# Optimization experiments

Hardware: AMD Instinct MI355X
Metric: run time of the kernel (lower is better)

The kernel has to match this reference:

```python
import jax, jax.numpy as jnp
import numpy as np

HEADS = 16

def setup_inputs() -> dict:
    key = jax.random.key(0)
    ks = jax.random.split(key, 5)
    B, N, D = 2, 2048, 1024
    q = jax.random.normal(ks[0], (B, N, D), dtype=jnp.float32)
    kv = jax.random.normal(ks[1], (B, N, D), dtype=jnp.float32)
    # nn.Linear default init scale ~ 1/sqrt(fan_in); use scaled normals
    s = 1.0 / np.sqrt(D)
    Wq = jax.random.normal(ks[2], (D, D), dtype=jnp.float32) * s
    Wkv = jax.random.normal(ks[3], (D, 2 * D), dtype=jnp.float32) * s
    Wout = jax.random.normal(ks[4], (D, D), dtype=jnp.float32) * s
    return {"q": q, "kv": kv, "Wq": Wq, "Wkv": Wkv, "Wout": Wout}

def reference(q, kv, Wq, Wkv, Wout):
    B, N, D = q.shape
    H = HEADS
    Dh = D // H
    scale = Dh ** -0.5
    # projections (Linear, no bias); weights stored [in, out]
    qp = q @ Wq                      # [B,N,D]
    kvp = kv @ Wkv                   # [B,N,2D]
    kp, vp = kvp[..., :D], kvp[..., D:]
    def split_heads(t):
        return t.reshape(B, N, H, Dh).transpose(0, 2, 1, 3)  # [B,H,N,Dh]
    qh, kh, vh = split_heads(qp), split_heads(kp), split_heads(vp)
    dots = jnp.einsum('bhid,bhjd->bhij', qh, kh) * scale
    # attn_fn = softmax computed in float32, cast back to input dtype
    attn = jax.nn.softmax(dots.astype(jnp.float32), axis=-1).astype(dots.dtype)
    out = jnp.einsum('bhij,bhjd->bhid', attn, vh)
    out = out.transpose(0, 2, 1, 3).reshape(B, N, D)
    return out @ Wout
```

## Files before the change

kernel.cpp:

```cpp
#include <hip/hip_runtime.h>
#include <hip/hip_fp16.h>
#include <stdint.h>

using u16 = unsigned short;
using f16   = _Float16;
using fp16v2 = __attribute__((ext_vector_type(2))) __fp16;
using f16x4 = __attribute__((ext_vector_type(4))) _Float16;
using f16x8 = __attribute__((ext_vector_type(8))) _Float16;
using f32x4 = __attribute__((ext_vector_type(4))) float;

__device__ __forceinline__ u16 f2h(float f) {
  union { f16 h; u16 u; } v;
  v.h = (f16)f;
  return v.u;
}

#define GLOBAL_LOAD_LDS16(gp, lp) \
  __builtin_amdgcn_global_load_lds((const __attribute__((address_space(1))) unsigned int*)(gp), \
                                   (__attribute__((address_space(3))) unsigned int*)(lp), 16, 0, 0)

#define MFMA32(a, b, c) __builtin_amdgcn_mfma_f32_16x16x32_f16(a, b, c, 0, 0, 0)
#define MFMA16(a, b, c) __builtin_amdgcn_mfma_f32_16x16x16f16(a, b, c, 0, 0, 0)

__global__ __launch_bounds__(256) void cast2_f16_k(const float4* __restrict__ a,
                                                   const float4* __restrict__ b,
                                                   u16* __restrict__ outa,
                                                   u16* __restrict__ outb, int n4each) {
  int i = blockIdx.x * 256 + threadIdx.x;
  const float4* src; u16* dst; int j;
  if (i < n4each) { src = a; dst = outa; j = i; }
  else            { src = b; dst = outb; j = i - n4each; }
  float4 f = src[j];
  ushort4 o;
  o.x = f2h(f.x); o.y = f2h(f.y); o.z = f2h(f.z); o.w = f2h(f.w);
  *(ushort4*)(dst + (size_t)j * 4) = o;
}

__global__ __launch_bounds__(256) void transpose3_k(const float* __restrict__ Wq,
                                                    const float* __restrict__ Wkv,
                                                    const float* __restrict__ Wout,
                                                    u16* __restrict__ WqT,
                                                    u16* __restrict__ WkvT,
                                                    u16* __restrict__ WoutT,
                                                    float qscale) {
  int blk = blockIdx.x;
  const float* in; u16* out; int t; float scale; int N;
  if (blk < 1024)      { in = Wq;   out = WqT;   t = blk;        scale = qscale; N = 1024; }
  else if (blk < 3072) { in = Wkv;  out = WkvT;  t = blk - 1024; scale = 1.0f;   N = 2048; }
  else                 { in = Wout; out = WoutT; t = blk - 3072; scale = 1.0f;   N = 1024; }
  const int K = 1024;
  __shared__ float tile[32][33];
  int bk = (t & 31) * 32, bn = (t >> 5) * 32;
  int tx = threadIdx.x & 31, ty = threadIdx.x >> 5;
#pragma unroll
  for (int i = 0; i < 4; i++) {
    int r = ty * 4 + i;
    tile[r][tx] = in[(size_t)(bk + r) * N + bn + tx];
  }
  __syncthreads();
#pragma unroll
  for (int i = 0; i < 4; i++) {
    int r = ty * 4 + i;
    out[(size_t)(bn + r) * K + bk + tx] = f2h(tile[tx][r] * scale);
  }
}

template <int BM, bool OUT_F32>
__device__ __forceinline__ void gemm_body(u16* lA, u16* lB,
                                          const u16* __restrict__ A, const u16* __restrict__ BT,
                                          void* __restrict__ Cv, int N, int K, int bm, int bn) {
  const int tid = threadIdx.x;
  const int lane = tid & 63, wave = tid >> 6;
  const int l15 = lane & 15, quad = lane >> 4;
  constexpr int MI = BM / 32;
  const int wm = (wave >> 1) * (BM / 2), wn = (wave & 1) * 64;

  f32x4 acc[MI][4] = {};

  const u16* Abase = A + (size_t)bm * BM * K;
  const u16* Bbase = BT + (size_t)bn * 128 * K;
  const int r0 = tid >> 2, c8 = (tid & 3) * 8;

  u16* lAw = lA + wave * 512;
  u16* lBw = lB + wave * 512;

  for (int k0 = 0; k0 < K; k0 += 32) {
    const u16* Ag = Abase + k0 + (size_t)r0 * K + c8;
    const u16* Bg = Bbase + k0 + (size_t)r0 * K + c8;
#pragma unroll
    for (int t = 0; t < BM / 64; t++)
      GLOBAL_LOAD_LDS16(Ag + (size_t)(t * 64) * K, lAw + t * 2048);
#pragma unroll
    for (int t = 0; t < 2; t++)
      GLOBAL_LOAD_LDS16(Bg + (size_t)(t * 64) * K, lBw + t * 2048);
    __syncthreads();

    f16x8 aF[MI], bF[4];
#pragma unroll
    for (int mi = 0; mi < MI; mi++)
      aF[mi] = *(const f16x8*)&lA[(wm + mi * 16 + l15) * 32 + quad * 8];
#pragma unroll
    for (int ni = 0; ni < 4; ni++)
      bF[ni] = *(const f16x8*)&lB[(wn + ni * 16 + l15) * 32 + quad * 8];
    __builtin_amdgcn_s_setprio(1);
#pragma unroll
    for (int mi = 0; mi < MI; mi++)
#pragma unroll
      for (int ni = 0; ni < 4; ni++)
        acc[mi][ni] = MFMA32(aF[mi], bF[ni], acc[mi][ni]);
    __builtin_amdgcn_s_setprio(0);
    __syncthreads();
  }

  const int col0 = bn * 128 + wn + l15;
  const int rowb = bm * BM + wm + quad * 4;
#pragma unroll
  for (int mi = 0; mi < MI; mi++) {
#pragma unroll
    for (int ni = 0; ni < 4; ni++) {
#pragma unroll
      for (int r = 0; r < 4; r++) {
        int row = rowb + mi * 16 + r;
        int col = col0 + ni * 16;
        float v = acc[mi][ni][r];
        if (OUT_F32) ((float*)Cv)[(size_t)row * N + col] = v;
        else         ((u16*)Cv)[(size_t)row * N + col] = f2h(v);
      }
    }
  }
}

__global__ __launch_bounds__(256) void proj_k(const u16* __restrict__ q16, const u16* __restrict__ WqT,
                                              u16* __restrict__ qp,
                                              const u16* __restrict__ kv16, const u16* __restrict__ WkvT,
                                              u16* __restrict__ kvp) {
  __shared__ u16 lA[128 * 32];
  __shared__ u16 lB[128 * 32];
  int blk = blockIdx.x;
  if (blk < 256) gemm_body<128, false>(lA, lB, q16, WqT, qp, 1024, 1024, blk >> 3, blk & 7);
  else { int b2 = blk - 256; gemm_body<128, false>(lA, lB, kv16, WkvT, kvp, 2048, 1024, b2 >> 4, b2 & 15); }
}

__global__ __launch_bounds__(256) void gemm_out_k(const u16* __restrict__ A, const u16* __restrict__ BT,
                                                  float* __restrict__ C) {
  __shared__ u16 lA[64 * 32];
  __shared__ u16 lB[128 * 32];
  int blk = blockIdx.x;
  gemm_body<64, true>(lA, lB, A, BT, C, 1024, 1024, blk >> 3, blk & 7);
}

__global__ __launch_bounds__(256) void vt_k(const u16* __restrict__ kvp,
                                            u16* __restrict__ VT) {
  __shared__ u16 lT[64 * 64];
  const int jt = blockIdx.x & 31;
  const int bh = blockIdx.x >> 5;
  const int b = bh >> 4, h = bh & 15;
  const int j0 = jt * 64;
  const int u = threadIdx.x;
  const int su = u >> 3;
  const int sc = (u & 7) * 8;

#pragma unroll
  for (int t = 0; t < 2; t++) {
    int j = su + t * 32;
    int s = (j ^ (j >> 3)) & 7;
    uint4 vv = *(const uint4*)(kvp + (size_t)(b * 2048 + j0 + j) * 2048 + 1024 + h * 64 + sc);
    *(uint4*)&lT[j * 64 + (sc ^ (s << 3))] = vv;
  }
  __syncthreads();

  const int jg = u & 7;
#pragma unroll
  for (int t = 0; t < 2; t++) {
    int d = su + t * 32;
    u16 tmp[8];
#pragma unroll
    for (int i = 0; i < 8; i++) {
      int j = jg * 8 + i;
      int s = (j ^ (j >> 3)) & 7;
      tmp[i] = lT[j * 64 + (d ^ (s << 3))];
    }
    *(uint4*)(VT + ((size_t)bh * 64 + d) * 2048 + j0 + jg * 8) = *(const uint4*)tmp;
  }
}

__global__ __launch_bounds__(256) void flash_attn_k(const u16* __restrict__ qp,
                                                    const u16* __restrict__ kvp,
                                                    const u16* __restrict__ VT,
                                                    u16* __restrict__ attn_out) {
  const int NSEQ = 2048, D = 1024, LDKV = 2048;
  const int mtile = blockIdx.x & 15;
  const int bh = blockIdx.x >> 4;
  const int b = bh >> 4, h = bh & 15;
  const int tid = threadIdx.x;
  const int lane = tid & 63, wave = tid >> 6;
  const int quad = lane >> 4, l15 = lane & 15;

  __shared__ u16 lK[2][128 * 64];
  __shared__ u16 lV[2][64 * 128];

  const u16* Qb  = qp + (size_t)(b * NSEQ + mtile * 128) * D + h * 64;
  const u16* Kb  = kvp + (size_t)(b * NSEQ) * LDKV + h * 64;
  const u16* VTb = VT + (size_t)bh * 64 * 2048;

  f16x8 qa[2][2];
#pragma unroll
  for (int qt = 0; qt < 2; qt++)
#pragma unroll
    for (int ks = 0; ks < 2; ks++)
      qa[qt][ks] = *(const f16x8*)(Qb + (size_t)(wave * 32 + qt * 16 + l15) * D + ks * 32 + quad * 8);

  f32x4 oacc[2][4] = {};
  float rs0 = 0.f, rs1 = 0.f;

#define STAGEB(LKB, LVB, J0)                                                        \
  {                                                                                 \
    u16* lKw_ = (LKB) + wave * 512;                                                 \
    u16* lVw_ = (LVB) + wave * 512;                                                 \
    _Pragma("unroll")                                                               \
    for (int t = 0; t < 4; t++) {                                                   \
      int g = t * 256 + tid;                                                        \
      int jr = g >> 3;                                                              \
      int c = (g & 7) ^ (jr & 7);                                                   \
      GLOBAL_LOAD_LDS16(Kb + (size_t)((J0) + jr) * LDKV + c * 8, lKw_ + t * 2048);  \
    }                                                                               \
    _Pragma("unroll")                                                               \
    for (int t = 0; t < 4; t++) {                                                   \
      int g = t * 256 + tid;                                                        \
      int d = g >> 4;                                                               \
      int c = (g & 15) ^ (d & 7);                                                   \
      GLOBAL_LOAD_LDS16(VTb + (size_t)d * 2048 + (J0) + c * 8, lVw_ + t * 2048);    \
    }                                                                               \
  }

  STAGEB(lK[0], lV[0], 0);

  for (int it = 0; it < 16; it++) {
    const int cur = it & 1;
    __syncthreads();
    if (it < 15) STAGEB(lK[cur ^ 1], lV[cur ^ 1], (it + 1) * 128);

    const u16* lKc = lK[cur];
    const u16* lVc = lV[cur];

#pragma unroll
    for (int ni = 0; ni < 8; ni++) {
      f32x4 s0 = f32x4{-4.f, -4.f, -4.f, -4.f};
      f32x4 s1 = s0;
      __builtin_amdgcn_s_setprio(1);
#pragma unroll
      for (int ks = 0; ks < 2; ks++) {
        int p = ((ks * 4 + quad) ^ (l15 & 7)) * 8;
        f16x8 kb = *(const f16x8*)&lKc[(ni * 16 + l15) * 64 + p];
        s0 = MFMA32(kb, qa[0][ks], s0);
        s1 = MFMA32(kb, qa[1][ks], s1);
      }
      __builtin_amdgcn_s_setprio(0);

      union { fp16v2 h2[2]; f16x4 v; } pa0, pa1;
      {
        float p0 = __builtin_amdgcn_exp2f(s0[0]);
        float p1 = __builtin_amdgcn_exp2f(s0[1]);
        float p2 = __builtin_amdgcn_exp2f(s0[2]);
        float p3 = __builtin_amdgcn_exp2f(s0[3]);
        rs0 += (p0 + p1) + (p2 + p3);
        pa0.h2[0] = __builtin_amdgcn_cvt_pkrtz(p0, p1);
        pa0.h2[1] = __builtin_amdgcn_cvt_pkrtz(p2, p3);
      }
      {
        float p0 = __builtin_amdgcn_exp2f(s1[0]);
        float p1 = __builtin_amdgcn_exp2f(s1[1]);
        float p2 = __builtin_amdgcn_exp2f(s1[2]);
        float p3 = __builtin_amdgcn_exp2f(s1[3]);
        rs1 += (p0 + p1) + (p2 + p3);
        pa1.h2[0] = __builtin_amdgcn_cvt_pkrtz(p0, p1);
        pa1.h2[1] = __builtin_amdgcn_cvt_pkrtz(p2, p3);
      }

      __builtin_amdgcn_s_setprio(1);
#pragma unroll
      for (int di = 0; di < 4; di++) {
        int p = (((2 * ni + (quad >> 1)) ^ (l15 & 7)) * 8) + (quad & 1) * 4;
        f16x4 vb = *(const f16x4*)&lVc[(di * 16 + l15) * 128 + p];
        oacc[0][di] = MFMA16(pa0.v, vb, oacc[0][di]);
        oacc[1][di] = MFMA16(pa1.v, vb, oacc[1][di]);
      }
      __builtin_amdgcn_s_setprio(0);
    }
  }

  rs0 += __shfl_xor(rs0, 16, 64);
  rs0 += __shfl_xor(rs0, 32, 64);
  rs1 += __shfl_xor(rs1, 16, 64);
  rs1 += __shfl_xor(rs1, 32, 64);
  float inv0 = 1.0f / rs0;
  float inv1 = 1.0f / rs1;
  float invq0[4], invq1[4];
#pragma unroll
  for (int r = 0; r < 4; r++) {
    int src = (lane & 48) + ((lane >> 4) << 2) + r;
    invq0[r] = __shfl(inv0, src, 64);
    invq1[r] = __shfl(inv1, src, 64);
  }

  u16* Ob = attn_out + (size_t)(b * NSEQ + mtile * 128) * D + h * 64;
#pragma unroll
  for (int di = 0; di < 4; di++)
#pragma unroll
    for (int r = 0; r < 4; r++) {
      float v0 = oacc[0][di][r] * invq0[r];
      float v1 = oacc[1][di][r] * invq1[r];
      Ob[(size_t)(wave * 32 + quad * 4 + r) * D + di * 16 + l15] = f2h(v0);
      Ob[(size_t)(wave * 32 + 16 + quad * 4 + r) * D + di * 16 + l15] = f2h(v1);
    }
}

extern "C" void kernel_launch(void* const* d_in, const int* in_sizes, int n_in,
                              void* d_out, int out_size, void* d_ws, size_t ws_size,
                              hipStream_t stream) {
  const float* q    = (const float*)d_in[0];
  const float* kv   = (const float*)d_in[1];
  const float* Wq   = (const float*)d_in[2];
  const float* Wkv  = (const float*)d_in[3];
  const float* Wout = (const float*)d_in[4];
  float* out = (float*)d_out;

  char* ws = (char*)d_ws;
  const size_t MB = 1024 * 1024;
  u16* q16   = (u16*)(ws + 0);
  u16* kv16  = (u16*)(ws + 8 * MB);
  u16* WqT   = (u16*)(ws + 16 * MB);
  u16* WkvT  = (u16*)(ws + 18 * MB);
  u16* WoutT = (u16*)(ws + 22 * MB);
  u16* qp    = (u16*)(ws + 24 * MB);
  u16* kvp   = (u16*)(ws + 32 * MB);
  u16* attn  = q16;
  u16* VT    = kv16;

  const float qscale = 0.125f * 1.44269504f;

  cast2_f16_k<<<8192, 256, 0, stream>>>((const float4*)q, (const float4*)kv,
                                        q16, kv16, 1048576);
  transpose3_k<<<4096, 256, 0, stream>>>(Wq, Wkv, Wout, WqT, WkvT, WoutT, qscale);

  proj_k<<<768, 256, 0, stream>>>(q16, WqT, qp, kv16, WkvT, kvp);
  vt_k<<<1024, 256, 0, stream>>>(kvp, VT);
  flash_attn_k<<<512, 256, 0, stream>>>(qp, kvp, VT, attn);
  gemm_out_k<<<512, 256, 0, stream>>>(attn, WoutT, out);
}
```

Measured before the change: 213.6 us.

## Fuse V transpose into KV projection epilogue and merge prep kernels

The KV projection GEMM now writes the V half directly in transposed per-head layout, which removes the separate vt_k kernel and its read and write of V. K is stored compactly with stride 1024. The cast and weight-transpose kernels are merged into a single launch, which removes one kernel launch. The s_setprio hints around the MFMA loop are dropped. The transposed V stores are 8-byte writes strided across rows, so they may coalesce poorly.

```diff
diff --git a/kernel.cpp b/kernel.cpp
--- a/kernel.cpp
+++ b/kernel.cpp
@@ -22,34 +22,34 @@
 #define MFMA32(a, b, c) __builtin_amdgcn_mfma_f32_16x16x32_f16(a, b, c, 0, 0, 0)
 #define MFMA16(a, b, c) __builtin_amdgcn_mfma_f32_16x16x16f16(a, b, c, 0, 0, 0)
 
-__global__ __launch_bounds__(256) void cast2_f16_k(const float4* __restrict__ a,
-                                                   const float4* __restrict__ b,
-                                                   u16* __restrict__ outa,
-                                                   u16* __restrict__ outb, int n4each) {
-  int i = blockIdx.x * 256 + threadIdx.x;
-  const float4* src; u16* dst; int j;
-  if (i < n4each) { src = a; dst = outa; j = i; }
-  else            { src = b; dst = outb; j = i - n4each; }
-  float4 f = src[j];
-  ushort4 o;
-  o.x = f2h(f.x); o.y = f2h(f.y); o.z = f2h(f.z); o.w = f2h(f.w);
-  *(ushort4*)(dst + (size_t)j * 4) = o;
-}
-
-__global__ __launch_bounds__(256) void transpose3_k(const float* __restrict__ Wq,
-                                                    const float* __restrict__ Wkv,
-                                                    const float* __restrict__ Wout,
-                                                    u16* __restrict__ WqT,
-                                                    u16* __restrict__ WkvT,
-                                                    u16* __restrict__ WoutT,
-                                                    float qscale) {
+__global__ __launch_bounds__(256) void prep_k(const float4* __restrict__ q,
+                                              const float4* __restrict__ kv,
+                                              u16* __restrict__ q16, u16* __restrict__ kv16,
+                                              const float* __restrict__ Wq,
+                                              const float* __restrict__ Wkv,
+                                              const float* __restrict__ Wout,
+                                              u16* __restrict__ WqT, u16* __restrict__ WkvT,
+                                              u16* __restrict__ WoutT, float qscale) {
+  __shared__ float tile[32][33];
   int blk = blockIdx.x;
+  if (blk < 8192) {
+    int i = blk * 256 + threadIdx.x;
+    const int n4each = 1048576;
+    const float4* src; u16* dst; int j;
+    if (i < n4each) { src = q;  dst = q16;  j = i; }
+    else            { src = kv; dst = kv16; j = i - n4each; }
+    float4 f = src[j];
+    ushort4 o;
+    o.x = f2h(f.x); o.y = f2h(f.y); o.z = f2h(f.z); o.w = f2h(f.w);
+    *(ushort4*)(dst + (size_t)j * 4) = o;
+    return;
+  }
+  int t2 = blk - 8192;
   const float* in; u16* out; int t; float scale; int N;
-  if (blk < 1024)      { in = Wq;   out = WqT;   t = blk;        scale = qscale; N = 1024; }
-  else if (blk < 3072) { in = Wkv;  out = WkvT;  t = blk - 1024; scale = 1.0f;   N = 2048; }
-  else                 { in = Wout; out = WoutT; t = blk - 3072; scale = 1.0f;   N = 1024; }
+  if (t2 < 1024)      { in = Wq;   out = WqT;   t = t2;        scale = qscale; N = 1024; }
+  else if (t2 < 3072) { in = Wkv;  out = WkvT;  t = t2 - 1024; scale = 1.0f;   N = 2048; }
+  else                { in = Wout; out = WoutT; t = t2 - 3072; scale = 1.0f;   N = 1024; }
   const int K = 1024;
-  __shared__ float tile[32][33];
   int bk = (t & 31) * 32, bn = (t >> 5) * 32;
   int tx = threadIdx.x & 31, ty = threadIdx.x >> 5;
 #pragma unroll
@@ -65,10 +65,11 @@
   }
 }
 
-template <int BM, bool OUT_F32>
+template <int BM, int MODE>
 __device__ __forceinline__ void gemm_body(u16* lA, u16* lB,
                                           const u16* __restrict__ A, const u16* __restrict__ BT,
-                                          void* __restrict__ Cv, int N, int K, int bm, int bn) {
+                                          void* __restrict__ Cv, u16* __restrict__ VTo,
+                                          int N, int K, int bm, int bn) {
   const int tid = threadIdx.x;
   const int lane = tid & 63, wave = tid >> 6;
   const int l15 = lane & 15, quad = lane >> 4;
@@ -102,18 +103,39 @@
 #pragma unroll
     for (int ni = 0; ni < 4; ni++)
       bF[ni] = *(const f16x8*)&lB[(wn + ni * 16 + l15) * 32 + quad * 8];
-    __builtin_amdgcn_s_setprio(1);
 #pragma unroll
     for (int mi = 0; mi < MI; mi++)
 #pragma unroll
       for (int ni = 0; ni < 4; ni++)
         acc[mi][ni] = MFMA32(aF[mi], bF[ni], acc[mi][ni]);
-    __builtin_amdgcn_s_setprio(0);
     __syncthreads();
   }
 
   const int col0 = bn * 128 + wn + l15;
   const int rowb = bm * BM + wm + quad * 4;
+
+  if (MODE == 2 && bn >= 8) {
+#pragma unroll
+    for (int mi = 0; mi < MI; mi++) {
+      int row0 = rowb + mi * 16;
+      int bb = row0 >> 11;
+      int j = row0 & 2047;
+#pragma unroll
+      for (int ni = 0; ni < 4; ni++) {
+        int c = col0 + ni * 16 - 1024;
+        int h = c >> 6, d = c & 63;
+        ushort4 o;
+        o.x = f2h(acc[mi][ni][0]);
+        o.y = f2h(acc[mi][ni][1]);
+        o.z = f2h(acc[mi][ni][2]);
+        o.w = f2h(acc[mi][ni][3]);
+        *(ushort4*)(VTo + ((size_t)((bb << 4) + h) * 64 + d) * 2048 + j) = o;
+      }
+    }
+    return;
+  }
+
+  const int cstride = (MODE == 2) ? 1024 : N;
 #pragma unroll
   for (int mi = 0; mi < MI; mi++) {
 #pragma unroll
@@ -123,8 +145,8 @@
         int row = rowb + mi * 16 + r;
         int col = col0 + ni * 16;
         float v = acc[mi][ni][r];
-        if (OUT_F32) ((float*)Cv)[(size_t)row * N + col] = v;
-        else         ((u16*)Cv)[(size_t)row * N + col] = f2h(v);
+        if (MODE == 1) ((float*)Cv)[(size_t)row * cstride + col] = v;
+        else           ((u16*)Cv)[(size_t)row * cstride + col] = f2h(v);
       }
     }
   }
@@ -133,12 +155,12 @@
 __global__ __launch_bounds__(256) void proj_k(const u16* __restrict__ q16, const u16* __restrict__ WqT,
                                               u16* __restrict__ qp,
                                               const u16* __restrict__ kv16, const u16* __restrict__ WkvT,
-                                              u16* __restrict__ kvp) {
+                                              u16* __restrict__ kvpK, u16* __restrict__ VT) {
   __shared__ u16 lA[128 * 32];
   __shared__ u16 lB[128 * 32];
   int blk = blockIdx.x;
-  if (blk < 256) gemm_body<128, false>(lA, lB, q16, WqT, qp, 1024, 1024, blk >> 3, blk & 7);
-  else { int b2 = blk - 256; gemm_body<128, false>(lA, lB, kv16, WkvT, kvp, 2048, 1024, b2 >> 4, b2 & 15); }
+  if (blk < 256) gemm_body<128, 0>(lA, lB, q16, WqT, qp, nullptr, 1024, 1024, blk >> 3, blk & 7);
+  else { int b2 = blk - 256; gemm_body<128, 2>(lA, lB, kv16, WkvT, kvpK, VT, 2048, 1024, b2 >> 4, b2 & 15); }
 }
 
 __global__ __launch_bounds__(256) void gemm_out_k(const u16* __restrict__ A, const u16* __restrict__ BT,
@@ -146,49 +168,14 @@
   __shared__ u16 lA[64 * 32];
   __shared__ u16 lB[128 * 32];
   int blk = blockIdx.x;
-  gemm_body<64, true>(lA, lB, A, BT, C, 1024, 1024, blk >> 3, blk & 7);
-}
-
-__global__ __launch_bounds__(256) void vt_k(const u16* __restrict__ kvp,
-                                            u16* __restrict__ VT) {
-  __shared__ u16 lT[64 * 64];
-  const int jt = blockIdx.x & 31;
-  const int bh = blockIdx.x >> 5;
-  const int b = bh >> 4, h = bh & 15;
-  const int j0 = jt * 64;
-  const int u = threadIdx.x;
-  const int su = u >> 3;
-  const int sc = (u & 7) * 8;
-
-#pragma unroll
-  for (int t = 0; t < 2; t++) {
-    int j = su + t * 32;
-    int s = (j ^ (j >> 3)) & 7;
-    uint4 vv = *(const uint4*)(kvp + (size_t)(b * 2048 + j0 + j) * 2048 + 1024 + h * 64 + sc);
-    *(uint4*)&lT[j * 64 + (sc ^ (s << 3))] = vv;
-  }
-  __syncthreads();
-
-  const int jg = u & 7;
-#pragma unroll
-  for (int t = 0; t < 2; t++) {
-    int d = su + t * 32;
-    u16 tmp[8];
-#pragma unroll
-    for (int i = 0; i < 8; i++) {
-      int j = jg * 8 + i;
-      int s = (j ^ (j >> 3)) & 7;
-      tmp[i] = lT[j * 64 + (d ^ (s << 3))];
-    }
-    *(uint4*)(VT + ((size_t)bh * 64 + d) * 2048 + j0 + jg * 8) = *(const uint4*)tmp;
-  }
+  gemm_body<64, 1>(lA, lB, A, BT, C, nullptr, 1024, 1024, blk >> 3, blk & 7);
 }
 
 __global__ __launch_bounds__(256) void flash_attn_k(const u16* __restrict__ qp,
-                                                    const u16* __restrict__ kvp,
+                                                    const u16* __restrict__ kvpK,
                                                     const u16* __restrict__ VT,
                                                     u16* __restrict__ attn_out) {
-  const int NSEQ = 2048, D = 1024, LDKV = 2048;
+  const int NSEQ = 2048, D = 1024, LDK = 1024;
   const int mtile = blockIdx.x & 15;
   const int bh = blockIdx.x >> 4;
   const int b = bh >> 4, h = bh & 15;
@@ -200,7 +187,7 @@
   __shared__ u16 lV[2][64 * 128];
 
   const u16* Qb  = qp + (size_t)(b * NSEQ + mtile * 128) * D + h * 64;
-  const u16* Kb  = kvp + (size_t)(b * NSEQ) * LDKV + h * 64;
+  const u16* Kb  = kvpK + (size_t)(b * NSEQ) * LDK + h * 64;
   const u16* VTb = VT + (size_t)bh * 64 * 2048;
 
   f16x8 qa[2][2];
@@ -222,7 +209,7 @@
       int g = t * 256 + tid;                                                        \
       int jr = g >> 3;                                                              \
       int c = (g & 7) ^ (jr & 7);                                                   \
-      GLOBAL_LOAD_LDS16(Kb + (size_t)((J0) + jr) * LDKV + c * 8, lKw_ + t * 2048);  \
+      GLOBAL_LOAD_LDS16(Kb + (size_t)((J0) + jr) * LDK + c * 8, lKw_ + t * 2048);   \
     }                                                                               \
     _Pragma("unroll")                                                               \
     for (int t = 0; t < 4; t++) {                                                   \
@@ -333,18 +320,15 @@
   u16* WkvT  = (u16*)(ws + 18 * MB);
   u16* WoutT = (u16*)(ws + 22 * MB);
   u16* qp    = (u16*)(ws + 24 * MB);
-  u16* kvp   = (u16*)(ws + 32 * MB);
+  u16* kvpK  = (u16*)(ws + 32 * MB);
+  u16* VT    = (u16*)(ws + 40 * MB);
   u16* attn  = q16;
-  u16* VT    = kv16;
 
   const float qscale = 0.125f * 1.44269504f;
 
-  cast2_f16_k<<<8192, 256, 0, stream>>>((const float4*)q, (const float4*)kv,
-                                        q16, kv16, 1048576);
-  transpose3_k<<<4096, 256, 0, stream>>>(Wq, Wkv, Wout, WqT, WkvT, WoutT, qscale);
-
-  proj_k<<<768, 256, 0, stream>>>(q16, WqT, qp, kv16, WkvT, kvp);
-  vt_k<<<1024, 256, 0, stream>>>(kvp, VT);
-  flash_attn_k<<<512, 256, 0, stream>>>(qp, kvp, VT, attn);
+  prep_k<<<12288, 256, 0, stream>>>((const float4*)q, (const float4*)kv, q16, kv16,
+                                    Wq, Wkv, Wout, WqT, WkvT, WoutT, qscale);
+  proj_k<<<768, 256, 0, stream>>>(q16, WqT, qp, kv16, WkvT, kvpK, VT);
+  flash_attn_k<<<512, 256, 0, stream>>>(qp, kvpK, VT, attn);
   gemm_out_k<<<512, 256, 0, stream>>>(attn, WoutT, out);
 }
```

Result: faster. 204.1 us (-4.4%).
